# Performance work log

Measured on AMD Instinct MI355X. Metric: run time of the kernel, lower is better.

Reference implementation:

```python
import jax, jax.numpy as jnp
import numpy as np

D_MODEL = 1024
NUM_HEADS = 16
HEAD_DIM = D_MODEL // NUM_HEADS


def setup_inputs() -> dict:
    key = jax.random.key(0)
    ks = jax.random.split(key, 10)
    B, SQ, SK = 2, 2048, 2048
    scale = 1.0 / np.sqrt(D_MODEL)
    inp = {
        "x1": jax.random.normal(ks[0], (B, SQ, D_MODEL), jnp.float32),
        "x2": jax.random.normal(ks[1], (B, SK, D_MODEL), jnp.float32),
        "Wq": jax.random.normal(ks[2], (D_MODEL, D_MODEL), jnp.float32) * scale,
        "bq": jnp.zeros((D_MODEL,), jnp.float32),
        "Wk": jax.random.normal(ks[3], (D_MODEL, D_MODEL), jnp.float32) * scale,
        "bk": jnp.zeros((D_MODEL,), jnp.float32),
        "Wv": jax.random.normal(ks[4], (D_MODEL, D_MODEL), jnp.float32) * scale,
        "bv": jnp.zeros((D_MODEL,), jnp.float32),
        "Wo": jax.random.normal(ks[5], (D_MODEL, D_MODEL), jnp.float32) * scale,
        "bo": jnp.zeros((D_MODEL,), jnp.float32),
    }
    return inp


def reference(x1, x2, Wq, bq, Wk, bk, Wv, bv, Wo, bo):
    B, SQ, _ = x1.shape
    SK = x2.shape[1]
    # projections, then split into heads: [B, H, S, Dh]
    def split_heads(t, S):
        return t.reshape(B, S, NUM_HEADS, HEAD_DIM).transpose(0, 2, 1, 3)
    Q = split_heads(x1 @ Wq + bq, SQ)
    K = split_heads(x2 @ Wk + bk, SK)
    V = split_heads(x2 @ Wv + bv, SK)
    # note: original scales by 1/head_dim**0.5
    scores = jnp.einsum("bhqd,bhkd->bhqk", Q, K) / jnp.sqrt(
        jnp.asarray(HEAD_DIM, Q.dtype))
    attn = jax.nn.softmax(scores, axis=-1)
    ctx = jnp.einsum("bhqk,bhkd->bhqd", attn, V)
    ctx = ctx.transpose(0, 2, 1, 3).reshape(B, SQ, D_MODEL)
    return ctx @ Wo + bo
```

## Files before the change

### kernel.cpp

```cpp
#include <hip/hip_runtime.h>
#include <stdint.h>


typedef unsigned short u16b;
typedef __attribute__((ext_vector_type(4))) short short4v;
typedef __attribute__((ext_vector_type(8))) short short8v;
typedef __attribute__((ext_vector_type(4))) float float4v;
typedef __attribute__((ext_vector_type(2))) unsigned int uint2v;

#if __has_builtin(__builtin_amdgcn_exp2f)
__device__ __forceinline__ float exp2_fast(float x){ return __builtin_amdgcn_exp2f(x); }
#else
__device__ __forceinline__ float exp2_fast(float x){ return exp2f(x); }
#endif

__device__ __forceinline__ u16b f2bf(float f) {
  union { float f; unsigned int i; } v; v.f = f;
  return (u16b)((v.i + 0x7fffu + ((v.i >> 16) & 1u)) >> 16);
}
__device__ __forceinline__ void gl_lds16(const u16b* g, u16b* l) {
  __builtin_amdgcn_global_load_lds(
      (const __attribute__((address_space(1))) void*)g,
      (__attribute__((address_space(3))) void*)l, 16, 0, 0);
}

__global__ __launch_bounds__(256) void prep(
    const float* __restrict__ x1, const float* __restrict__ x2,
    const float* __restrict__ W0, const float* __restrict__ W1,
    const float* __restrict__ W2, const float* __restrict__ W3,
    u16b* __restrict__ x1b, u16b* __restrict__ x2b, u16b* __restrict__ WT) {
  const int tid = threadIdx.x;
  const int mode = blockIdx.y;
  if (mode < 2) {
    const float* src = mode ? x2 : x1;
    u16b* dst = mode ? x2b : x1b;
    const int n4 = 1024*1024;
    int i = blockIdx.x * 256 + tid;
    const int stride = gridDim.x * 256;
    for (; i < n4; i += stride) {
      float4v v = ((const float4v*)src)[i];
      short4v o;
      o[0]=(short)f2bf(v[0]); o[1]=(short)f2bf(v[1]);
      o[2]=(short)f2bf(v[2]); o[3]=(short)f2bf(v[3]);
      ((short4v*)dst)[i] = o;
    }
  } else {
    __shared__ u16b tile[32][33];
    const int z = mode - 2;
    const float* src = (z==0) ? W0 : (z==1) ? W1 : (z==2) ? W2 : W3;
    u16b* dst = WT + (size_t)z * (1024*1024);
    const int x = tid & 31, y = tid >> 5;
    const int bx = (blockIdx.x & 31) * 32, by = (blockIdx.x >> 5) * 32;
#pragma unroll
    for (int j=0;j<4;++j)
      tile[y*4+j][x] = f2bf(src[(size_t)(by + y*4+j)*1024 + bx + x]);
    __syncthreads();
#pragma unroll
    for (int j=0;j<4;++j)
      dst[(size_t)(bx + y*4+j)*1024 + by + x] = tile[x][y*4+j];
  }
}

template<int BN, bool OUT_F32, bool BIAS_ROW>
__device__ __forceinline__ void gemm_core(
    u16b* __restrict__ As, u16b* __restrict__ Bs,
    const u16b* __restrict__ A, const u16b* __restrict__ Bt,
    const float* __restrict__ bias, void* __restrict__ Cv,
    int N, int K, int bm, int bn, float oscale) {
  constexpr int NT = BN / 32;
  const int tid = threadIdx.x;
  const int lane = tid & 63, wave = tid >> 6;
  const int wm = wave >> 1, wn = wave & 1;
  const int l15 = lane & 15, l4 = lane >> 4;
  float4v acc[4][NT];
#pragma unroll
  for (int i=0;i<4;++i)
#pragma unroll
    for (int j=0;j<NT;++j) acc[i][j] = (float4v){0.f,0.f,0.f,0.f};

  const int swz = (l15 >> 1) & 3;

  for (int k0 = 0; k0 < K; k0 += 32) {
    __syncthreads();
    {
      int row = tid >> 2, seg = tid & 3;
      int segg0 = seg ^ ((row >> 1) & 3);
      int row2 = row + 64;
      int segg1 = seg ^ ((row2 >> 1) & 3);
      gl_lds16(&A[(size_t)(bm+row )*K + k0 + segg0*8], &As[tid*8]);
      gl_lds16(&A[(size_t)(bm+row2)*K + k0 + segg1*8], &As[(tid+256)*8]);
      gl_lds16(&Bt[(size_t)(bn+row )*K + k0 + segg0*8], &Bs[tid*8]);
      if (BN == 128)
        gl_lds16(&Bt[(size_t)(bn+row2)*K + k0 + segg1*8], &Bs[(tid+256)*8]);
    }
    __syncthreads();
    short8v af[4], bf[NT];
#pragma unroll
    for (int mt=0;mt<4;++mt)
      af[mt] = *(const short8v*)&As[(wm*64+mt*16+l15)*32 + ((l4 ^ swz)*8)];
#pragma unroll
    for (int nt=0;nt<NT;++nt)
      bf[nt] = *(const short8v*)&Bs[(wn*(BN/2)+nt*16+l15)*32 + ((l4 ^ swz)*8)];
#pragma unroll
    for (int mt=0;mt<4;++mt)
#pragma unroll
      for (int nt=0;nt<NT;++nt)
        acc[mt][nt] = __builtin_amdgcn_mfma_f32_16x16x32_bf16(af[mt], bf[nt], acc[mt][nt], 0, 0, 0);
  }

#pragma unroll
  for (int nt=0;nt<NT;++nt) {
    int col = bn + wn*(BN/2) + nt*16 + l15;
    float bbc = BIAS_ROW ? 0.f : bias[col];
#pragma unroll
    for (int mt=0;mt<4;++mt) {
      int row0 = bm + wm*64 + mt*16 + l4*4;
#pragma unroll
      for (int r=0;r<4;++r) {
        float bb = BIAS_ROW ? bias[row0+r] : bbc;
        float v = (acc[mt][nt][r] + bb) * oscale;
        if (OUT_F32) ((float*)Cv)[(size_t)(row0+r)*N + col] = v;
        else         ((u16b*)Cv)[(size_t)(row0+r)*N + col] = f2bf(v);
      }
    }
  }
}

__global__ __launch_bounds__(256) void gemm_qkv(
    const u16b* __restrict__ x1b, const u16b* __restrict__ x2b,
    const u16b* __restrict__ WT, const float* __restrict__ bq,
    const float* __restrict__ bk, const float* __restrict__ bv,
    u16b* __restrict__ QKV) {
  __shared__ __align__(16) u16b As[128*32];
  __shared__ __align__(16) u16b Bs[128*32];
  const int z = blockIdx.z;
  const size_t Mi = 1024*1024;
  const float QSCALE = 0.125f * 1.4426950408889634f;
  if (z == 2) {
    gemm_core<128,false,true>(As, Bs, WT + 2*Mi, x2b, bv, QKV + 8*Mi,
                              4096, 1024, blockIdx.x*128, blockIdx.y*128, 1.0f);
  } else {
    gemm_core<128,false,false>(As, Bs, z ? x2b : x1b, WT + (size_t)z*Mi,
                               z ? bk : bq, QKV + (size_t)z*4*Mi,
                               1024, 1024, blockIdx.y*128, blockIdx.x*128,
                               z ? 1.0f : QSCALE);
  }
}

__global__ __launch_bounds__(256) void gemm_out(
    const u16b* __restrict__ A, const u16b* __restrict__ Bt,
    const float* __restrict__ bias, float* __restrict__ C) {
  __shared__ __align__(16) u16b As[128*32];
  __shared__ __align__(16) u16b Bs[64*32];
  gemm_core<64,true,false>(As, Bs, A, Bt, bias, C, 1024, 1024,
                           blockIdx.y*128, blockIdx.x*64, 1.0f);
}

__global__ __launch_bounds__(256, 2) void attn_q128(
    const u16b* __restrict__ Q, const u16b* __restrict__ Kg,
    const u16b* __restrict__ Vt, u16b* __restrict__ O) {
  __shared__ __align__(16) u16b Ks[128*64];
  __shared__ __align__(16) u16b Vs[64*128];
  __shared__ __align__(16) u16b Ps[4*2*1024];
  const int tid = threadIdx.x;
  const int lane = tid & 63, wave = tid >> 6;
  const int l15 = lane & 15, l4 = lane >> 4;
  const int bh = blockIdx.x;
  const int b = bh >> 4, h = bh & 15;
  const int q0 = blockIdx.y * 128;
  const size_t seqbase = (size_t)b * 2048;
  const int colh = h * 64;
  u16b* Pw = Ps + wave * 2048;

  short8v qf[2][2];
#pragma unroll
  for (int g=0; g<2; ++g) {
    size_t qrow = seqbase + q0 + wave*32 + g*16 + l15;
#pragma unroll
    for (int ks=0; ks<2; ++ks)
      qf[g][ks] = *(const short8v*)&Q[qrow*1024 + colh + ks*32 + l4*8];
  }

  short8v ones;
#pragma unroll
  for (int i=0;i<8;++i) ones[i] = (short)0x3F80;

  float4v lacc[2] = {(float4v){0.f,0.f,0.f,0.f}, (float4v){0.f,0.f,0.f,0.f}};
  float4v oacc[2][4];
#pragma unroll
  for (int g=0; g<2; ++g)
#pragma unroll
    for (int nb=0; nb<4; ++nb) oacc[g][nb] = (float4v){0.f,0.f,0.f,0.f};

  for (int kt = 0; kt < 16; ++kt) {
    const size_t kvbase = seqbase + (size_t)kt*128;
    __syncthreads();
#pragma unroll
    for (int j=0; j<4; ++j) {
      int idx = j*256 + tid;
      {
        int row = idx >> 3, seg = idx & 7;
        gl_lds16(&Kg[(kvbase+row)*1024 + colh + ((seg ^ (row & 7))*8)], &Ks[idx*8]);
      }
      {
        int row = idx >> 4, seg = idx & 15;
        gl_lds16(&Vt[(size_t)(h*64+row)*4096 + (size_t)b*2048 + kt*128
                     + ((seg ^ (row & 15))*8)], &Vs[idx*8]);
      }
    }
    __syncthreads();

    float4v sacc[2][8];
#pragma unroll
    for (int g=0; g<2; ++g)
#pragma unroll
      for (int nb=0; nb<8; ++nb) sacc[g][nb] = (float4v){0.f,0.f,0.f,0.f};
#pragma unroll
    for (int nb=0; nb<8; ++nb)
#pragma unroll
      for (int ks=0; ks<2; ++ks) {
        short8v kf = *(const short8v*)&Ks[(nb*16+l15)*64 + (((ks*4+l4) ^ (l15 & 7))*8)];
        sacc[0][nb] = __builtin_amdgcn_mfma_f32_16x16x32_bf16(kf, qf[0][ks], sacc[0][nb], 0, 0, 0);
        sacc[1][nb] = __builtin_amdgcn_mfma_f32_16x16x32_bf16(kf, qf[1][ks], sacc[1][nb], 0, 0, 0);
      }

#pragma unroll
    for (int h2=0; h2<2; ++h2) {
#pragma unroll
      for (int g=0; g<2; ++g)
#pragma unroll
        for (int nbl=0; nbl<4; ++nbl) {
          const float4v s4 = sacc[g][h2*4 + nbl];
          unsigned int u0 = __float_as_uint(exp2_fast(s4[0]));
          unsigned int u1 = __float_as_uint(exp2_fast(s4[1]));
          unsigned int u2 = __float_as_uint(exp2_fast(s4[2]));
          unsigned int u3 = __float_as_uint(exp2_fast(s4[3]));
          uint2v dw;
          dw[0] = (u0 >> 16) | (u1 & 0xFFFF0000u);
          dw[1] = (u2 >> 16) | (u3 & 0xFFFF0000u);
          *(uint2v*)&Pw[g*1024 + l15*64 + (((nbl*4 + l4) ^ l15)*4)] = dw;
        }
      __asm__ __volatile__("s_waitcnt lgkmcnt(0)" ::: "memory");

#pragma unroll
      for (int ks2=0; ks2<2; ++ks2) {
        short8v pf[2];
#pragma unroll
        for (int g=0; g<2; ++g) {
          int c0 = (ks2*8 + l4*2) ^ l15;
          int c1 = (ks2*8 + l4*2 + 1) ^ l15;
          short4v pa = *(const short4v*)&Pw[g*1024 + l15*64 + c0*4];
          short4v pb = *(const short4v*)&Pw[g*1024 + l15*64 + c1*4];
          short8v p;
          p[0]=pa[0]; p[1]=pa[1]; p[2]=pa[2]; p[3]=pa[3];
          p[4]=pb[0]; p[5]=pb[1]; p[6]=pb[2]; p[7]=pb[3];
          pf[g] = p;
          lacc[g] = __builtin_amdgcn_mfma_f32_16x16x32_bf16(p, ones, lacc[g], 0, 0, 0);
        }
#pragma unroll
        for (int nb=0; nb<4; ++nb) {
          int cc = (h2*8 + ks2*4 + l4) ^ l15;
          short8v vf = *(const short8v*)&Vs[(nb*16+l15)*128 + cc*8];
          oacc[0][nb] = __builtin_amdgcn_mfma_f32_16x16x32_bf16(pf[0], vf, oacc[0][nb], 0, 0, 0);
          oacc[1][nb] = __builtin_amdgcn_mfma_f32_16x16x32_bf16(pf[1], vf, oacc[1][nb], 0, 0, 0);
        }
      }
    }
  }

#pragma unroll
  for (int g=0; g<2; ++g)
#pragma unroll
    for (int r=0; r<4; ++r) {
      float inv = 1.0f / lacc[g][r];
      size_t row = seqbase + q0 + wave*32 + g*16 + l4*4 + r;
#pragma unroll
      for (int nb=0; nb<4; ++nb)
        O[row*1024 + colh + nb*16 + l15] = f2bf(oacc[g][nb][r] * inv);
    }
}

extern "C" void kernel_launch(void* const* d_in, const int* in_sizes, int n_in,
                              void* d_out, int out_size, void* d_ws, size_t ws_size,
                              hipStream_t stream) {
  const float* x1 = (const float*)d_in[0];
  const float* x2 = (const float*)d_in[1];
  const float* Wq = (const float*)d_in[2];
  const float* bq = (const float*)d_in[3];
  const float* Wk = (const float*)d_in[4];
  const float* bk = (const float*)d_in[5];
  const float* Wv = (const float*)d_in[6];
  const float* bv = (const float*)d_in[7];
  const float* Wo = (const float*)d_in[8];
  const float* bo = (const float*)d_in[9];
  (void)in_sizes; (void)n_in; (void)out_size; (void)ws_size;

  u16b* ws = (u16b*)d_ws;
  const size_t Mi = 1024*1024;
  u16b* WT  = ws;
  u16b* WoT = ws + 3*Mi;
  u16b* x1b = ws + 4*Mi;
  u16b* x2b = ws + 8*Mi;
  u16b* QKV = ws + 12*Mi;
  u16b* Qb  = QKV;
  u16b* Kb  = QKV + 4*Mi;
  u16b* Vtb = QKV + 8*Mi;
  u16b* Cx  = x1b;

  prep<<<dim3(1024,6), 256, 0, stream>>>(x1, x2, Wq, Wk, Wv, Wo, x1b, x2b, WT);

  gemm_qkv<<<dim3(8,32,3), 256, 0, stream>>>(x1b, x2b, WT, bq, bk, bv, QKV);

  attn_q128<<<dim3(32,16), 256, 0, stream>>>(Qb, Kb, Vtb, Cx);

  gemm_out<<<dim3(16,32), 256, 0, stream>>>(Cx, WoT, bo, (float*)d_out);
}
```

Before: 216.8 us.

## Deepen GEMM K-tile to 64 and remap blocks for XCD locality

The GEMM core now stages 64-wide K slices per iteration with an 8-way XOR swizzle and runs two MFMA sub-steps per slice. This halves the number of barrier pairs per K loop. Both GEMM launches become 1D grids whose block index is decoded so that each XCD (index mod 8) gets a contiguous band of M rows, to improve L2 reuse across the chiplets. LDS use per block doubles, which may reduce occupancy.

New measurement: 206.7 us. 4.7% less time.

```diff
diff --git a/kernel.cpp b/kernel.cpp
--- a/kernel.cpp
+++ b/kernel.cpp
@@ -78,34 +78,39 @@
 #pragma unroll
     for (int j=0;j<NT;++j) acc[i][j] = (float4v){0.f,0.f,0.f,0.f};
 
-  const int swz = (l15 >> 1) & 3;
-
-  for (int k0 = 0; k0 < K; k0 += 32) {
-    __syncthreads();
-    {
-      int row = tid >> 2, seg = tid & 3;
-      int segg0 = seg ^ ((row >> 1) & 3);
-      int row2 = row + 64;
-      int segg1 = seg ^ ((row2 >> 1) & 3);
-      gl_lds16(&A[(size_t)(bm+row )*K + k0 + segg0*8], &As[tid*8]);
-      gl_lds16(&A[(size_t)(bm+row2)*K + k0 + segg1*8], &As[(tid+256)*8]);
-      gl_lds16(&Bt[(size_t)(bn+row )*K + k0 + segg0*8], &Bs[tid*8]);
-      if (BN == 128)
-        gl_lds16(&Bt[(size_t)(bn+row2)*K + k0 + segg1*8], &Bs[(tid+256)*8]);
-    }
-    __syncthreads();
-    short8v af[4], bf[NT];
-#pragma unroll
-    for (int mt=0;mt<4;++mt)
-      af[mt] = *(const short8v*)&As[(wm*64+mt*16+l15)*32 + ((l4 ^ swz)*8)];
-#pragma unroll
-    for (int nt=0;nt<NT;++nt)
-      bf[nt] = *(const short8v*)&Bs[(wn*(BN/2)+nt*16+l15)*32 + ((l4 ^ swz)*8)];
-#pragma unroll
-    for (int mt=0;mt<4;++mt)
+  for (int k0 = 0; k0 < K; k0 += 64) {
+    __syncthreads();
+#pragma unroll
+    for (int j=0;j<4;++j) {
+      int idx = j*256 + tid;
+      int row = idx >> 3, seg = idx & 7;
+      int segg = seg ^ (row & 7);
+      gl_lds16(&A[(size_t)(bm+row)*K + k0 + segg*8], &As[idx*8]);
+    }
+#pragma unroll
+    for (int j=0;j<BN/32;++j) {
+      int idx = j*256 + tid;
+      int row = idx >> 3, seg = idx & 7;
+      int segg = seg ^ (row & 7);
+      gl_lds16(&Bt[(size_t)(bn+row)*K + k0 + segg*8], &Bs[idx*8]);
+    }
+    __syncthreads();
+#pragma unroll
+    for (int ks=0; ks<2; ++ks) {
+      short8v af[4], bf[NT];
+      const int cs = ((ks*4 + l4) ^ (l15 & 7)) * 8;
+#pragma unroll
+      for (int mt=0;mt<4;++mt)
+        af[mt] = *(const short8v*)&As[(wm*64+mt*16+l15)*64 + cs];
 #pragma unroll
       for (int nt=0;nt<NT;++nt)
-        acc[mt][nt] = __builtin_amdgcn_mfma_f32_16x16x32_bf16(af[mt], bf[nt], acc[mt][nt], 0, 0, 0);
+        bf[nt] = *(const short8v*)&Bs[(wn*(BN/2)+nt*16+l15)*64 + cs];
+#pragma unroll
+      for (int mt=0;mt<4;++mt)
+#pragma unroll
+        for (int nt=0;nt<NT;++nt)
+          acc[mt][nt] = __builtin_amdgcn_mfma_f32_16x16x32_bf16(af[mt], bf[nt], acc[mt][nt], 0, 0, 0);
+    }
   }
 
 #pragma unroll
@@ -131,29 +136,37 @@
     const u16b* __restrict__ WT, const float* __restrict__ bq,
     const float* __restrict__ bk, const float* __restrict__ bv,
     u16b* __restrict__ QKV) {
-  __shared__ __align__(16) u16b As[128*32];
-  __shared__ __align__(16) u16b Bs[128*32];
-  const int z = blockIdx.z;
+  __shared__ __align__(16) u16b As[128*64];
+  __shared__ __align__(16) u16b Bs[128*64];
+  const int f = blockIdx.x;
+  const int xcd = f & 7, s = f >> 3;
+  const int z = s >> 5, t = s & 31;
   const size_t Mi = 1024*1024;
   const float QSCALE = 0.125f * 1.4426950408889634f;
   if (z == 2) {
+    int bm = (t & 7) * 128;
+    int bn = (xcd*4 + (t >> 3)) * 128;
     gemm_core<128,false,true>(As, Bs, WT + 2*Mi, x2b, bv, QKV + 8*Mi,
-                              4096, 1024, blockIdx.x*128, blockIdx.y*128, 1.0f);
+                              4096, 1024, bm, bn, 1.0f);
   } else {
+    int bm = (xcd*4 + (t >> 3)) * 128;
+    int bn = (t & 7) * 128;
     gemm_core<128,false,false>(As, Bs, z ? x2b : x1b, WT + (size_t)z*Mi,
                                z ? bk : bq, QKV + (size_t)z*4*Mi,
-                               1024, 1024, blockIdx.y*128, blockIdx.x*128,
-                               z ? 1.0f : QSCALE);
+                               1024, 1024, bm, bn, z ? 1.0f : QSCALE);
   }
 }
 
 __global__ __launch_bounds__(256) void gemm_out(
     const u16b* __restrict__ A, const u16b* __restrict__ Bt,
     const float* __restrict__ bias, float* __restrict__ C) {
-  __shared__ __align__(16) u16b As[128*32];
-  __shared__ __align__(16) u16b Bs[64*32];
-  gemm_core<64,true,false>(As, Bs, A, Bt, bias, C, 1024, 1024,
-                           blockIdx.y*128, blockIdx.x*64, 1.0f);
+  __shared__ __align__(16) u16b As[128*64];
+  __shared__ __align__(16) u16b Bs[64*64];
+  const int f = blockIdx.x;
+  const int xcd = f & 7, s = f >> 3;
+  const int bm = (xcd*4 + (s >> 4)) * 128;
+  const int bn = (s & 15) * 64;
+  gemm_core<64,true,false>(As, Bs, A, Bt, bias, C, 1024, 1024, bm, bn, 1.0f);
 }
 
 __global__ __launch_bounds__(256, 2) void attn_q128(
@@ -309,9 +322,9 @@
 
   prep<<<dim3(1024,6), 256, 0, stream>>>(x1, x2, Wq, Wk, Wv, Wo, x1b, x2b, WT);
 
-  gemm_qkv<<<dim3(8,32,3), 256, 0, stream>>>(x1b, x2b, WT, bq, bk, bv, QKV);
+  gemm_qkv<<<dim3(768), 256, 0, stream>>>(x1b, x2b, WT, bq, bk, bv, QKV);
 
   attn_q128<<<dim3(32,16), 256, 0, stream>>>(Qb, Kb, Vtb, Cx);
 
-  gemm_out<<<dim3(16,32), 256, 0, stream>>>(Cx, WoT, bo, (float*)d_out);
-}
+  gemm_out<<<dim3(512), 256, 0, stream>>>(Cx, WoT, bo, (float*)d_out);
+}
```
